# Performance work log

Measured on AMD Instinct MI355X. Metric: run time of the kernel, lower is better.

The kernel has to match this reference:

```python
import jax, jax.numpy as jnp
import numpy as np

B, D, HGT, WID = 32, 512, 8, 32   # batch, channels, feature map H, W
T = HGT * WID                     # 256 spatial tokens
NH, L, MAXLEN = 8, 2, 25          # heads, encoder layers, max text len


def _ln(x, s, b, eps=1e-5):
    m = jnp.mean(x, -1, keepdims=True)
    v = jnp.mean((x - m) ** 2, -1, keepdims=True)
    return (x - m) * jax.lax.rsqrt(v + eps) * s + b


def setup_inputs() -> dict:
    key = jax.random.key(0)
    ks = jax.random.split(key, 16)
    w = lambda k, shp: jax.random.normal(k, shp, jnp.float32) * 0.02
    return {
        "x": jax.random.normal(ks[0], (B, D, HGT, WID), jnp.float32),
        "encoder_word_pos": jnp.arange(T, dtype=jnp.int32),
        "gsrm_word_pos": jnp.arange(MAXLEN, dtype=jnp.int32),
        # encoder positional table
        "pos_table": w(ks[1], (T, D)),
        # per-layer encoder params (stacked over L)
        "ln1_s": jnp.ones((L, D), jnp.float32), "ln1_b": jnp.zeros((L, D), jnp.float32),
        "Wq": w(ks[2], (L, D, D)), "bq": jnp.zeros((L, D), jnp.float32),
        "Wk": w(ks[3], (L, D, D)), "bk": jnp.zeros((L, D), jnp.float32),
        "Wv": w(ks[4], (L, D, D)), "bv": jnp.zeros((L, D), jnp.float32),
        "Wo": w(ks[5], (L, D, D)), "bo": jnp.zeros((L, D), jnp.float32),
        "ln2_s": jnp.ones((L, D), jnp.float32), "ln2_b": jnp.zeros((L, D), jnp.float32),
        "W1": w(ks[6], (L, D, D)), "b1": jnp.zeros((L, D), jnp.float32),  # d_inner_hid = hidden_dim
        "W2": w(ks[7], (L, D, D)), "b2": jnp.zeros((L, D), jnp.float32),
        "lnf_s": jnp.ones((D,), jnp.float32), "lnf_b": jnp.zeros((D,), jnp.float32),
        # PVAM head params
        "fc0_w": w(ks[8], (D, D)), "fc0_b": jnp.zeros((D,), jnp.float32),
        "emb_table": w(ks[9], (MAXLEN, D)),
        "fc1_w": w(ks[10], (D,)),
    }


def _pvam(x, encoder_word_pos, gsrm_word_pos, pos_table,
          ln1_s, ln1_b, Wq, bq, Wk, bk, Wv, bv, Wo, bo,
          ln2_s, ln2_b, W1, b1, W2, b2, lnf_s, lnf_b,
          fc0_w, fc0_b, emb_table, fc1_w):
    b, c, h, wd = x.shape
    feat = x.reshape(b, c, h * wd).transpose(0, 2, 1)          # [b, t, c]
    # prepare encoder: scale + learned positional embedding (eval mode: no dropout)
    enc = feat * jnp.sqrt(jnp.float32(c)) + pos_table[encoder_word_pos]
    dk = c // NH
    scale = 1.0 / jnp.sqrt(jnp.float32(dk))
    for l in range(L):  # pre-norm transformer encoder (preprocess='n', postprocess='da')
        qin = _ln(enc, ln1_s[l], ln1_b[l])
        q = (qin @ Wq[l] + bq[l]).reshape(b, -1, NH, dk)
        k = (qin @ Wk[l] + bk[l]).reshape(b, -1, NH, dk)
        v = (qin @ Wv[l] + bv[l]).reshape(b, -1, NH, dk)
        p = jax.nn.softmax(jnp.einsum('bqhd,bkhd->bhqk', q, k) * scale, -1)
        o = jnp.einsum('bhqk,bkhd->bqhd', p, v).reshape(b, -1, c)
        enc = enc + (o @ Wo[l] + bo[l])
        y = _ln(enc, ln2_s[l], ln2_b[l])
        enc = enc + (jax.nn.relu(y @ W1[l] + b1[l]) @ W2[l] + b2[l])
    enc = _ln(enc, lnf_s, lnf_b)
    word_features = enc @ fc0_w + fc0_b                        # [b, t, c]
    word_pos = emb_table[gsrm_word_pos]                        # [max_len, c]
    # additive attention: tanh(broadcast add) -> scalar score -> softmax over t
    y = jnp.tanh(word_features[:, None, :, :] + word_pos[None, :, None, :])  # [b,max_len,t,c]
    attn = jax.nn.softmax(jnp.einsum('bmtc,c->bmt', y, fc1_w), -1)
    return jnp.einsum('bmt,btc->bmc', attn, word_features)    # [b, max_len, c]


def reference(x, encoder_word_pos, gsrm_word_pos, pos_table,
              ln1_s, ln1_b, Wq, bq, Wk, bk, Wv, bv, Wo, bo,
              ln2_s, ln2_b, W1, b1, W2, b2, lnf_s, lnf_b,
              fc0_w, fc0_b, emb_table, fc1_w):
    return _pvam(x, encoder_word_pos, gsrm_word_pos, pos_table,
                 ln1_s, ln1_b, Wq, bq, Wk, bk, Wv, bv, Wo, bo,
                 ln2_s, ln2_b, W1, b1, W2, b2, lnf_s, lnf_b,
                 fc0_w, fc0_b, emb_table, fc1_w)
```

## Files before the change

### kernel.cpp

```cpp
#include <hip/hip_runtime.h>
#include <math.h>

#define B_ 32
#define D_ 512
#define T_ 256
#define NH_ 8
#define DK_ 64
#define ML_ 25

typedef unsigned short ushort_t;
using short8 = __attribute__((ext_vector_type(8))) short;
using f32x4  = __attribute__((ext_vector_type(4))) float;

__device__ __forceinline__ ushort_t f2bf(float f) {
    unsigned u = __float_as_uint(f);
    unsigned r = (u + 0x7fffu + ((u >> 16) & 1u)) >> 16;
    return (ushort_t)r;
}
__device__ __forceinline__ float bf2f(ushort_t h) {
    return __uint_as_float(((unsigned)h) << 16);
}
__device__ __forceinline__ void gl16(const void* g, void* l) {
    __builtin_amdgcn_global_load_lds((const __attribute__((address_space(1))) void*)g,
                                     (__attribute__((address_space(3))) void*)l, 16, 0, 0);
}
#define ZERO4(v) { (v)[0]=0.f; (v)[1]=0.f; (v)[2]=0.f; (v)[3]=0.f; }

__global__ __launch_bounds__(256) void prep_kernel(const float* __restrict__ x,
                                                   const int* __restrict__ epos,
                                                   const float* __restrict__ pos,
                                                   float* __restrict__ enc) {
    __shared__ float ld[64][65];
    int tt = blockIdx.x, ct = blockIdx.y, b = blockIdx.z;
    int t0 = tt * 64, c0 = ct * 64;
    int tid = threadIdx.x;
    int r = tid >> 4, c4 = (tid & 15) << 2;
#pragma unroll
    for (int p = 0; p < 4; p++) {
        int row = p * 16 + r;
        float4 v = *(const float4*)(x + ((size_t)(b * D_ + c0 + row) * T_ + t0) + c4);
        ld[row][c4 + 0] = v.x; ld[row][c4 + 1] = v.y; ld[row][c4 + 2] = v.z; ld[row][c4 + 3] = v.w;
    }
    __syncthreads();
#pragma unroll
    for (int p = 0; p < 4; p++) {
        int tr = p * 16 + r;
        int ep = epos[t0 + tr];
        float4 pv = *(const float4*)(pos + (size_t)ep * D_ + c0 + c4);
        float4 o;
        o.x = ld[c4 + 0][tr] * 22.627417f + pv.x;
        o.y = ld[c4 + 1][tr] * 22.627417f + pv.y;
        o.z = ld[c4 + 2][tr] * 22.627417f + pv.z;
        o.w = ld[c4 + 3][tr] * 22.627417f + pv.w;
        *(float4*)(enc + (size_t)(b * T_ + t0 + tr) * D_ + c0 + c4) = o;
    }
}

__global__ __launch_bounds__(256) void convert_w_kernel(const float* __restrict__ Wq,
                                                        const float* __restrict__ Wk,
                                                        const float* __restrict__ Wv,
                                                        const float* __restrict__ Wo,
                                                        const float* __restrict__ W1,
                                                        const float* __restrict__ W2,
                                                        const float* __restrict__ fc0,
                                                        ushort_t* __restrict__ wt) {
    __shared__ float ld[64][65];
    int m = blockIdx.x >> 6;
    int tile = blockIdx.x & 63;
    int tn = tile >> 3, tk = tile & 7;
    int n0 = tn * 64, k0 = tk * 64;
    const float* src;
    if (m < 12) {
        int l = m / 6, w = m % 6;
        const float* bases[6] = {Wq, Wk, Wv, Wo, W1, W2};
        src = bases[w] + (size_t)l * D_ * D_;
    } else {
        src = fc0;
    }
    int tid = threadIdx.x;
    int r = tid >> 4, c4 = (tid & 15) << 2;
#pragma unroll
    for (int p = 0; p < 4; p++) {
        int row = p * 16 + r;
        float4 v = *(const float4*)(src + (size_t)(k0 + row) * D_ + n0 + c4);
        ld[row][c4 + 0] = v.x; ld[row][c4 + 1] = v.y; ld[row][c4 + 2] = v.z; ld[row][c4 + 3] = v.w;
    }
    __syncthreads();
    ushort_t* dsth = wt + (size_t)m * D_ * D_;
    ushort_t* dstl = wt + (size_t)13 * D_ * D_;
#pragma unroll
    for (int p = 0; p < 4; p++) {
        int n = p * 16 + r;
        int kc = c4;
        ushort_t h[4], lo[4];
#pragma unroll
        for (int i = 0; i < 4; i++) {
            float f = ld[kc + i][n];
            h[i] = f2bf(f);
            lo[i] = f2bf(f - bf2f(h[i]));
        }
        *(ushort4*)(dsth + (size_t)(n0 + n) * D_ + k0 + kc) = make_ushort4(h[0], h[1], h[2], h[3]);
        if (m == 12)
            *(ushort4*)(dstl + (size_t)(n0 + n) * D_ + k0 + kc) = make_ushort4(lo[0], lo[1], lo[2], lo[3]);
    }
}

template<bool LO>
__global__ __launch_bounds__(256) void ln_kernel(const float* __restrict__ x,
                                                 const float* __restrict__ s,
                                                 const float* __restrict__ b,
                                                 ushort_t* __restrict__ yh,
                                                 ushort_t* __restrict__ yl) {
    int wid = threadIdx.x >> 6, lane = threadIdx.x & 63;
    size_t row = (size_t)blockIdx.x * 4 + wid;
    const float4* xr = (const float4*)(x + row * D_);
    float4 v0 = xr[lane * 2], v1 = xr[lane * 2 + 1];
    float sum = v0.x + v0.y + v0.z + v0.w + v1.x + v1.y + v1.z + v1.w;
    for (int o = 32; o; o >>= 1) sum += __shfl_xor(sum, o);
    float mean = sum * (1.f / 512.f);
    float d[8] = {v0.x - mean, v0.y - mean, v0.z - mean, v0.w - mean,
                  v1.x - mean, v1.y - mean, v1.z - mean, v1.w - mean};
    float vs = 0.f;
#pragma unroll
    for (int i = 0; i < 8; i++) vs += d[i] * d[i];
    for (int o = 32; o; o >>= 1) vs += __shfl_xor(vs, o);
    float rs = 1.f / sqrtf(vs * (1.f / 512.f) + 1e-5f);
    const float4* s4 = (const float4*)s;
    const float4* b4 = (const float4*)b;
    float4 sa = s4[lane * 2], sb = s4[lane * 2 + 1];
    float4 ba = b4[lane * 2], bb = b4[lane * 2 + 1];
    float o8[8];
    o8[0] = d[0] * rs * sa.x + ba.x; o8[1] = d[1] * rs * sa.y + ba.y;
    o8[2] = d[2] * rs * sa.z + ba.z; o8[3] = d[3] * rs * sa.w + ba.w;
    o8[4] = d[4] * rs * sb.x + bb.x; o8[5] = d[5] * rs * sb.y + bb.y;
    o8[6] = d[6] * rs * sb.z + bb.z; o8[7] = d[7] * rs * sb.w + bb.w;
    ushort_t h[8];
#pragma unroll
    for (int i = 0; i < 8; i++) h[i] = f2bf(o8[i]);
    uint4 u;
    u.x = (unsigned)h[0] | ((unsigned)h[1] << 16);
    u.y = (unsigned)h[2] | ((unsigned)h[3] << 16);
    u.z = (unsigned)h[4] | ((unsigned)h[5] << 16);
    u.w = (unsigned)h[6] | ((unsigned)h[7] << 16);
    *(uint4*)(yh + row * D_ + lane * 8) = u;
    if (LO) {
        ushort_t l8[8];
#pragma unroll
        for (int i = 0; i < 8; i++) l8[i] = f2bf(o8[i] - bf2f(h[i]));
        uint4 ul;
        ul.x = (unsigned)l8[0] | ((unsigned)l8[1] << 16);
        ul.y = (unsigned)l8[2] | ((unsigned)l8[3] << 16);
        ul.z = (unsigned)l8[4] | ((unsigned)l8[5] << 16);
        ul.w = (unsigned)l8[6] | ((unsigned)l8[7] << 16);
        *(uint4*)(yl + row * D_ + lane * 8) = ul;
    }
}

template<int EPI>
__global__ __launch_bounds__(256) void gemm_kernel(const ushort_t* __restrict__ A0,
                                                   const ushort_t* __restrict__ A1,
                                                   const ushort_t* __restrict__ A2,
                                                   const ushort_t* __restrict__ B0,
                                                   const ushort_t* __restrict__ B1,
                                                   const ushort_t* __restrict__ B2,
                                                   int nseg, int nbn,
                                                   const float* __restrict__ bias,
                                                   const float* __restrict__ bias2,
                                                   const float* __restrict__ bias3,
                                                   const float* __restrict__ res,
                                                   float* __restrict__ outF,
                                                   ushort_t* __restrict__ outB) {
    __shared__ ushort_t As[3][64 * 64];
    __shared__ ushort_t Bs[3][64 * 64];
    int tid = threadIdx.x;
    int g = blockIdx.x;
    int per = gridDim.x >> 3;
    int lin = (g & 7) * per + (g >> 3);
    int bm = lin / nbn, bn = lin % nbn;

    int lane = tid & 63;
    int wid = tid >> 6;
    int wm = wid >> 1, wn = wid & 1;
    int xr = (lane & 7) << 3;

    f32x4 acc[2][2];
#pragma unroll
    for (int i = 0; i < 2; i++)
#pragma unroll
        for (int j = 0; j < 2; j++) ZERO4(acc[i][j]);

    int nt = nseg * 8;

#define STAGE(kt, buf)                                                                  \
    {                                                                                   \
        int seg_ = (kt) >> 3;                                                           \
        int k0_ = ((kt) & 7) * 64;                                                      \
        const ushort_t* Asg = seg_ == 0 ? A0 : (seg_ == 1 ? A1 : A2);                   \
        const ushort_t* Bsg = seg_ == 0 ? B0 : (seg_ == 1 ? B1 : B2);                   \
        _Pragma("unroll")                                                               \
        for (int it = 0; it < 2; it++) {                                                \
            int uu = tid + it * 256;                                                    \
            int row_ = uu >> 3;                                                         \
            int kb_ = (((uu & 7) ^ (row_ & 7)) << 3);                                   \
            gl16(Asg + (size_t)(bm * 64 + row_) * 512 + k0_ + kb_, &As[buf][uu * 8]);   \
        }                                                                               \
        _Pragma("unroll")                                                               \
        for (int it = 0; it < 2; it++) {                                                \
            int uu = tid + it * 256;                                                    \
            int row_ = uu >> 3;                                                         \
            int kb_ = (((uu & 7) ^ (row_ & 7)) << 3);                                   \
            gl16(Bsg + (size_t)(bn * 64 + row_) * 512 + k0_ + kb_, &Bs[buf][uu * 8]);   \
        }                                                                               \
    }

#define COMPUTE(bufc)                                                                        \
    {                                                                                        \
        _Pragma("unroll")                                                                    \
        for (int kc = 0; kc < 2; kc++) {                                                     \
            short8 a[2], b[2];                                                               \
            int koff = (kc * 32 + ((lane >> 4) << 3)) ^ xr;                                  \
            _Pragma("unroll")                                                                \
            for (int i = 0; i < 2; i++)                                                      \
                a[i] = *(const short8*)&As[bufc][(wm * 32 + i * 16 + (lane & 15)) * 64 + koff]; \
            _Pragma("unroll")                                                                \
            for (int j = 0; j < 2; j++)                                                      \
                b[j] = *(const short8*)&Bs[bufc][(wn * 32 + j * 16 + (lane & 15)) * 64 + koff]; \
            _Pragma("unroll")                                                                \
            for (int i = 0; i < 2; i++)                                                      \
                _Pragma("unroll")                                                            \
                for (int j = 0; j < 2; j++)                                                  \
                    acc[i][j] = __builtin_amdgcn_mfma_f32_16x16x32_bf16(a[i], b[j], acc[i][j], 0, 0, 0); \
        }                                                                                    \
    }

    STAGE(0, 0);
    STAGE(1, 1);
    asm volatile("s_waitcnt vmcnt(4)" ::: "memory");
    __builtin_amdgcn_s_barrier();

    int cur = 0;
    for (int t = 0; t < nt; t++) {
        if (t + 2 < nt) STAGE(t + 2, (cur + 2 >= 3 ? cur - 1 : cur + 2));
        COMPUTE(cur);
        if (t + 2 < nt) {
            asm volatile("s_waitcnt vmcnt(4)" ::: "memory");
        } else if (t + 1 < nt) {
            asm volatile("s_waitcnt vmcnt(0)" ::: "memory");
        }
        __builtin_amdgcn_s_barrier();
        cur = (cur == 2) ? 0 : cur + 1;
    }
#undef STAGE
#undef COMPUTE

#pragma unroll
    for (int i = 0; i < 2; i++) {
#pragma unroll
        for (int j = 0; j < 2; j++) {
            int r0 = bm * 64 + wm * 32 + i * 16 + ((lane >> 4) << 2);
            int col = bn * 64 + wn * 32 + j * 16 + (lane & 15);
            int seg = col >> 9;
            int ccol = col & 511;
            const float* bp = bias;
            if (EPI == 5) bp = (seg == 0) ? bias : (seg == 1 ? bias2 : bias3);
            float bc = bp[EPI == 5 ? ccol : col];
#pragma unroll
            for (int jj = 0; jj < 4; jj++) {
                float v = acc[i][j][jj] + bc;
                int row = r0 + jj;
                size_t idx = (size_t)row * 512 + col;
                if (EPI == 2) {
                    outF[idx] = v + res[idx];
                } else if (EPI == 3) {
                    outB[idx] = f2bf(fmaxf(v, 0.f));
                } else if (EPI == 4) {
                    outF[idx] = v;
                } else if (EPI == 5) {
                    if (seg < 2) {
                        outB[(size_t)seg * 4194304 + (size_t)row * 512 + ccol] = f2bf(v);
                    } else {
                        int bb2 = row >> 8, t2 = row & 255;
                        outB[(size_t)2 * 4194304 +
                             ((size_t)(bb2 * 8 + (ccol >> 6)) * 64 + (ccol & 63)) * 256 + t2] = f2bf(v);
                    }
                }
            }
        }
    }
}

__global__ __launch_bounds__(256) void attn_fused_kernel(const ushort_t* __restrict__ q,
                                                         const ushort_t* __restrict__ k,
                                                         const ushort_t* __restrict__ vt,
                                                         ushort_t* __restrict__ ao) {
    __shared__ ushort_t KVs[256 * 64];
    __shared__ ushort_t Ps[64 * 256];
    int tid = threadIdx.x;
    int lane = tid & 63;
    int wid = tid >> 6;
    int m0 = blockIdx.x * 64;
    int bh = blockIdx.y;
    int b = bh >> 3, h = bh & 7;
    int xr = (lane & 7) << 3;

#pragma unroll
    for (int it = 0; it < 8; it++) {
        int uu = tid + it * 256;
        int row = uu >> 3;
        int gx = ((uu & 7) ^ (row & 7)) << 3;
        gl16(k + (size_t)(b * T_ + row) * D_ + h * DK_ + gx, &KVs[uu * 8]);
    }
    short8 qa0, qa1;
    {
        int qrow = m0 + wid * 16 + (lane & 15);
        const ushort_t* qp = q + (size_t)(b * T_ + qrow) * D_ + h * DK_ + ((lane >> 4) << 3);
        qa0 = *(const short8*)(qp);
        qa1 = *(const short8*)(qp + 32);
    }
    f32x4 acc[16];
#pragma unroll
    for (int j = 0; j < 16; j++) ZERO4(acc[j]);
    asm volatile("s_waitcnt vmcnt(0)" ::: "memory");
    __syncthreads();

#pragma unroll
    for (int j = 0; j < 16; j++) {
        int krow = j * 16 + (lane & 15);
        short8 b0 = *(const short8*)&KVs[krow * 64 + ((((lane >> 4) << 3)) ^ xr)];
        short8 b1 = *(const short8*)&KVs[krow * 64 + ((32 + ((lane >> 4) << 3)) ^ xr)];
        acc[j] = __builtin_amdgcn_mfma_f32_16x16x32_bf16(qa0, b0, acc[j], 0, 0, 0);
        acc[j] = __builtin_amdgcn_mfma_f32_16x16x32_bf16(qa1, b1, acc[j], 0, 0, 0);
    }
    __syncthreads();

#pragma unroll
    for (int it = 0; it < 8; it++) {
        int uu = tid + it * 256;
        int row = uu >> 5;
        int gx = ((uu & 31) ^ (row & 7)) << 3;
        gl16(vt + ((size_t)bh * DK_ + row) * T_ + gx, &KVs[uu * 8]);
    }

    const float C = 0.125f * 1.44269504f;
#pragma unroll
    for (int jj = 0; jj < 4; jj++) {
        float mx = -1e30f;
#pragma unroll
        for (int j = 0; j < 16; j++) mx = fmaxf(mx, acc[j][jj]);
#pragma unroll
        for (int msk = 1; msk < 16; msk <<= 1) mx = fmaxf(mx, __shfl_xor(mx, msk));
        float sm = 0.f;
#pragma unroll
        for (int j = 0; j < 16; j++) {
            float e = __builtin_amdgcn_exp2f((acc[j][jj] - mx) * C);
            acc[j][jj] = e;
            sm += e;
        }
#pragma unroll
        for (int msk = 1; msk < 16; msk <<= 1) sm += __shfl_xor(sm, msk);
        float inv = 1.f / sm;
#pragma unroll
        for (int j = 0; j < 16; j++) acc[j][jj] *= inv;
    }
#pragma unroll
    for (int j = 0; j < 16; j++) {
#pragma unroll
        for (int jj = 0; jj < 4; jj++) {
            int row = wid * 16 + ((lane >> 4) << 2) + jj;
            int col = j * 16 + (lane & 15);
            Ps[row * 256 + (col ^ ((row & 7) << 3))] = f2bf(acc[j][jj]);
        }
    }
    asm volatile("s_waitcnt vmcnt(0)" ::: "memory");
    __syncthreads();

    int wm = wid >> 1, wn = wid & 1;
    f32x4 acc2[2][2];
#pragma unroll
    for (int i = 0; i < 2; i++)
#pragma unroll
        for (int j = 0; j < 2; j++) ZERO4(acc2[i][j]);
#pragma unroll
    for (int kc = 0; kc < 8; kc++) {
        int off = (kc * 32 + ((lane >> 4) << 3)) ^ xr;
        short8 a0 = *(const short8*)&Ps[(wm * 32 + (lane & 15)) * 256 + off];
        short8 a1 = *(const short8*)&Ps[(wm * 32 + 16 + (lane & 15)) * 256 + off];
        short8 b0 = *(const short8*)&KVs[(wn * 32 + (lane & 15)) * 256 + off];
        short8 b1 = *(const short8*)&KVs[(wn * 32 + 16 + (lane & 15)) * 256 + off];
        acc2[0][0] = __builtin_amdgcn_mfma_f32_16x16x32_bf16(a0, b0, acc2[0][0], 0, 0, 0);
        acc2[0][1] = __builtin_amdgcn_mfma_f32_16x16x32_bf16(a0, b1, acc2[0][1], 0, 0, 0);
        acc2[1][0] = __builtin_amdgcn_mfma_f32_16x16x32_bf16(a1, b0, acc2[1][0], 0, 0, 0);
        acc2[1][1] = __builtin_amdgcn_mfma_f32_16x16x32_bf16(a1, b1, acc2[1][1], 0, 0, 0);
    }
#pragma unroll
    for (int i = 0; i < 2; i++)
#pragma unroll
        for (int j = 0; j < 2; j++)
#pragma unroll
            for (int jj = 0; jj < 4; jj++)
                ao[(size_t)(b * T_ + m0 + wm * 32 + i * 16 + ((lane >> 4) << 2) + jj) * D_ +
                   h * DK_ + wn * 32 + j * 16 + (lane & 15)] = f2bf(acc2[i][j][jj]);
}

__global__ __launch_bounds__(256) void scores_kernel(const float* __restrict__ wf,
                                                     const int* __restrict__ gpos,
                                                     const float* __restrict__ emb,
                                                     const float* __restrict__ w1,
                                                     float* __restrict__ scores) {
    __shared__ float wpL[5][512];
    __shared__ float w1m2[512];
    const float K2 = 2.885390082f;
    int tid = threadIdx.x;
    int b = blockIdx.y;
    int mg = blockIdx.z * 5;
    int t = blockIdx.x * 32 + (tid >> 3);
    int cg = tid & 7;
    for (int idx = tid; idx < 5 * 128; idx += 256) {
        int m = idx >> 7, w4 = idx & 127;
        float4 v = *(const float4*)(emb + (size_t)gpos[mg + m] * D_ + (w4 << 2));
        v.x *= K2; v.y *= K2; v.z *= K2; v.w *= K2;
        *(float4*)&wpL[m][w4 << 2] = v;
    }
    if (tid < 128) {
        float4 v = *(const float4*)(w1 + (tid << 2));
        v.x *= -2.f; v.y *= -2.f; v.z *= -2.f; v.w *= -2.f;
        *(float4*)&w1m2[tid << 2] = v;
    }
    float4 wfs[16];
    float W1S = 0.f;
    const float* wfr = wf + (size_t)(b * T_ + t) * D_ + (cg << 2);
#pragma unroll
    for (int j = 0; j < 16; j++) {
        float4 v = *(const float4*)(wfr + (j << 5));
        wfs[j].x = v.x * K2; wfs[j].y = v.y * K2; wfs[j].z = v.z * K2; wfs[j].w = v.w * K2;
        float4 wv = *(const float4*)(w1 + (cg << 2) + (j << 5));
        W1S += wv.x + wv.y + wv.z + wv.w;
    }
    __syncthreads();
    float s[5] = {W1S, W1S, W1S, W1S, W1S};
#pragma unroll
    for (int j = 0; j < 16; j++) {
        float4 w14 = *(const float4*)&w1m2[(cg << 2) + (j << 5)];
#pragma unroll
        for (int m = 0; m < 5; m++) {
            float4 wp4 = *(const float4*)&wpL[m][(cg << 2) + (j << 5)];
            s[m] += w14.x * __builtin_amdgcn_rcpf(__builtin_amdgcn_exp2f(wfs[j].x + wp4.x) + 1.f);
            s[m] += w14.y * __builtin_amdgcn_rcpf(__builtin_amdgcn_exp2f(wfs[j].y + wp4.y) + 1.f);
            s[m] += w14.z * __builtin_amdgcn_rcpf(__builtin_amdgcn_exp2f(wfs[j].z + wp4.z) + 1.f);
            s[m] += w14.w * __builtin_amdgcn_rcpf(__builtin_amdgcn_exp2f(wfs[j].w + wp4.w) + 1.f);
        }
    }
#pragma unroll
    for (int m = 0; m < 5; m++) {
        s[m] += __shfl_xor(s[m], 1);
        s[m] += __shfl_xor(s[m], 2);
        s[m] += __shfl_xor(s[m], 4);
    }
    if (cg == 0) {
#pragma unroll
        for (int m = 0; m < 5; m++)
            scores[((size_t)b * ML_ + mg + m) * T_ + t] = s[m];
    }
}

__global__ __launch_bounds__(256) void wsum_kernel(const float* __restrict__ scores,
                                                   const float* __restrict__ wf,
                                                   float* __restrict__ out) {
    __shared__ float at[T_][8];
    __shared__ float redmax[4][8];
    __shared__ float redsum[4][8];
    int tid = threadIdx.x;
    int lane = tid & 63, wv = tid >> 6;
    int b = blockIdx.y, m0 = blockIdx.x * 5;
    float s[5];
#pragma unroll
    for (int q = 0; q < 5; q++)
        s[q] = scores[((size_t)b * ML_ + m0 + q) * T_ + tid];
#pragma unroll
    for (int q = 0; q < 5; q++) {
        float mx = s[q];
        for (int o = 32; o; o >>= 1) mx = fmaxf(mx, __shfl_xor(mx, o));
        if (lane == 0) redmax[wv][q] = mx;
    }
    __syncthreads();
    float e[5];
#pragma unroll
    for (int q = 0; q < 5; q++) {
        float m = fmaxf(fmaxf(redmax[0][q], redmax[1][q]), fmaxf(redmax[2][q], redmax[3][q]));
        e[q] = __expf(s[q] - m);
        float sm = e[q];
        for (int o = 32; o; o >>= 1) sm += __shfl_xor(sm, o);
        if (lane == 0) redsum[wv][q] = sm;
    }
    __syncthreads();
#pragma unroll
    for (int q = 0; q < 5; q++) {
        float sm = redsum[0][q] + redsum[1][q] + redsum[2][q] + redsum[3][q];
        at[tid][q] = e[q] / sm;
    }
    __syncthreads();
    int c0 = tid << 1;
    const float* wfb = wf + (size_t)b * T_ * D_ + c0;
    float acc[5][2] = {};
    for (int t = 0; t < T_; t++) {
        float2 v = *(const float2*)(wfb + (size_t)t * D_);
        float4 a4 = *(const float4*)&at[t][0];
        float a5 = at[t][4];
        acc[0][0] += a4.x * v.x; acc[0][1] += a4.x * v.y;
        acc[1][0] += a4.y * v.x; acc[1][1] += a4.y * v.y;
        acc[2][0] += a4.z * v.x; acc[2][1] += a4.z * v.y;
        acc[3][0] += a4.w * v.x; acc[3][1] += a4.w * v.y;
        acc[4][0] += a5 * v.x;   acc[4][1] += a5 * v.y;
    }
#pragma unroll
    for (int q = 0; q < 5; q++) {
        float2 o;
        o.x = acc[q][0]; o.y = acc[q][1];
        *(float2*)(out + ((size_t)b * ML_ + m0 + q) * D_ + c0) = o;
    }
}

extern "C" void kernel_launch(void* const* d_in, const int* in_sizes, int n_in,
                              void* d_out, int out_size, void* d_ws, size_t ws_size,
                              hipStream_t stream) {
    (void)in_sizes; (void)n_in; (void)out_size; (void)ws_size;
    const float* x        = (const float*)d_in[0];
    const int*   epos     = (const int*)d_in[1];
    const int*   gpos     = (const int*)d_in[2];
    const float* pos_tab  = (const float*)d_in[3];
    const float* ln1_s    = (const float*)d_in[4];
    const float* ln1_b    = (const float*)d_in[5];
    const float* Wq       = (const float*)d_in[6];
    const float* bq       = (const float*)d_in[7];
    const float* Wk       = (const float*)d_in[8];
    const float* bk       = (const float*)d_in[9];
    const float* Wv       = (const float*)d_in[10];
    const float* bv       = (const float*)d_in[11];
    const float* Wo       = (const float*)d_in[12];
    const float* bo       = (const float*)d_in[13];
    const float* ln2_s    = (const float*)d_in[14];
    const float* ln2_b    = (const float*)d_in[15];
    const float* W1       = (const float*)d_in[16];
    const float* b1       = (const float*)d_in[17];
    const float* W2       = (const float*)d_in[18];
    const float* b2       = (const float*)d_in[19];
    const float* lnf_s    = (const float*)d_in[20];
    const float* lnf_b    = (const float*)d_in[21];
    const float* fc0_w    = (const float*)d_in[22];
    const float* fc0_b    = (const float*)d_in[23];
    const float* emb      = (const float*)d_in[24];
    const float* fc1_w    = (const float*)d_in[25];

    char* ws = (char*)d_ws;
    float*    enc = (float*)(ws);
    ushort_t* hi  = (ushort_t*)(ws + 16777216);
    ushort_t* qb  = (ushort_t*)(ws + 25165824);
    ushort_t* kb  = (ushort_t*)(ws + 33554432);
    ushort_t* lo  = (ushort_t*)(ws + 33554432);
    float*    scb = (float*)(ws + 33554432);
    ushort_t* vt  = (ushort_t*)(ws + 41943040);
    ushort_t* h1  = (ushort_t*)(ws + 41943040);
    ushort_t* ao  = (ushort_t*)(ws + 50331648);
    float*    wf  = (float*)(ws + 58720256);
    ushort_t* wt  = (ushort_t*)(ws + 75497472);
    const size_t WSL = (size_t)D_ * D_;

    convert_w_kernel<<<13 * 64, 256, 0, stream>>>(Wq, Wk, Wv, Wo, W1, W2, fc0_w, wt);
    prep_kernel<<<dim3(4, 8, 32), 256, 0, stream>>>(x, epos, pos_tab, enc);

    for (int l = 0; l < 2; l++) {
        size_t o1 = (size_t)l * D_;
        const ushort_t* WqkvT = wt + (l * 6 + 0) * WSL;
        const ushort_t* WoT = wt + (l * 6 + 3) * WSL;
        const ushort_t* W1T = wt + (l * 6 + 4) * WSL;
        const ushort_t* W2T = wt + (l * 6 + 5) * WSL;

        ln_kernel<false><<<2048, 256, 0, stream>>>(enc, ln1_s + o1, ln1_b + o1, hi, nullptr);
        gemm_kernel<5><<<3072, 256, 0, stream>>>(hi, nullptr, nullptr, WqkvT, nullptr, nullptr,
                                                 1, 24, bq + o1, bk + o1, bv + o1, nullptr, nullptr, qb);
        attn_fused_kernel<<<dim3(4, 256), 256, 0, stream>>>(qb, kb, vt, ao);
        gemm_kernel<2><<<1024, 256, 0, stream>>>(ao, nullptr, nullptr, WoT, nullptr, nullptr,
                                                 1, 8, bo + o1, nullptr, nullptr, enc, enc, nullptr);
        ln_kernel<false><<<2048, 256, 0, stream>>>(enc, ln2_s + o1, ln2_b + o1, hi, nullptr);
        gemm_kernel<3><<<1024, 256, 0, stream>>>(hi, nullptr, nullptr, W1T, nullptr, nullptr,
                                                 1, 8, b1 + o1, nullptr, nullptr, nullptr, nullptr, h1);
        gemm_kernel<2><<<1024, 256, 0, stream>>>(h1, nullptr, nullptr, W2T, nullptr, nullptr,
                                                 1, 8, b2 + o1, nullptr, nullptr, enc, enc, nullptr);
    }

    ln_kernel<true><<<2048, 256, 0, stream>>>(enc, lnf_s, lnf_b, hi, lo);
    gemm_kernel<4><<<1024, 256, 0, stream>>>(hi, lo, hi, wt + 12 * WSL, wt + 12 * WSL, wt + 13 * WSL,
                                             3, 8, fc0_b, nullptr, nullptr, nullptr, wf, nullptr);
    scores_kernel<<<dim3(8, 32, 5), 256, 0, stream>>>(wf, gpos, emb, fc1_w, scb);
    wsum_kernel<<<dim3(5, 32), 256, 0, stream>>>(scb, wf, (float*)d_out);
}
```

Baseline: 313.1 us.

## Enlarge GEMM tiles to 128-row blocks and add dedicated 128x128 QKV kernel

The generic GEMM tile grows from 64x64 to 128x64, so each wave computes 64x32 outputs and the grid is halved. A new QKV projection kernel uses 128x128 tiles with double buffering and keeps the bias selection and V-transpose epilogue. Larger tiles raise reuse of each loaded operand and cut global and LDS traffic per FLOP. In exchange they use more LDS and registers per block and launch fewer blocks, which may lower occupancy and leave fewer blocks to spread across CUs.

```diff
diff --git a/kernel.cpp b/kernel.cpp
--- a/kernel.cpp
+++ b/kernel.cpp
@@ -165,12 +165,10 @@
                                                    const ushort_t* __restrict__ B2,
                                                    int nseg, int nbn,
                                                    const float* __restrict__ bias,
-                                                   const float* __restrict__ bias2,
-                                                   const float* __restrict__ bias3,
                                                    const float* __restrict__ res,
                                                    float* __restrict__ outF,
                                                    ushort_t* __restrict__ outB) {
-    __shared__ ushort_t As[3][64 * 64];
+    __shared__ ushort_t As[3][128 * 64];
     __shared__ ushort_t Bs[3][64 * 64];
     int tid = threadIdx.x;
     int g = blockIdx.x;
@@ -183,9 +181,9 @@
     int wm = wid >> 1, wn = wid & 1;
     int xr = (lane & 7) << 3;
 
-    f32x4 acc[2][2];
-#pragma unroll
-    for (int i = 0; i < 2; i++)
+    f32x4 acc[4][2];
+#pragma unroll
+    for (int i = 0; i < 4; i++)
 #pragma unroll
         for (int j = 0; j < 2; j++) ZERO4(acc[i][j]);
 
@@ -198,11 +196,11 @@
         const ushort_t* Asg = seg_ == 0 ? A0 : (seg_ == 1 ? A1 : A2);                   \
         const ushort_t* Bsg = seg_ == 0 ? B0 : (seg_ == 1 ? B1 : B2);                   \
         _Pragma("unroll")                                                               \
-        for (int it = 0; it < 2; it++) {                                                \
+        for (int it = 0; it < 4; it++) {                                                \
             int uu = tid + it * 256;                                                    \
             int row_ = uu >> 3;                                                         \
             int kb_ = (((uu & 7) ^ (row_ & 7)) << 3);                                   \
-            gl16(Asg + (size_t)(bm * 64 + row_) * 512 + k0_ + kb_, &As[buf][uu * 8]);   \
+            gl16(Asg + (size_t)(bm * 128 + row_) * 512 + k0_ + kb_, &As[buf][uu * 8]);  \
         }                                                                               \
         _Pragma("unroll")                                                               \
         for (int it = 0; it < 2; it++) {                                                \
@@ -217,16 +215,16 @@
     {                                                                                        \
         _Pragma("unroll")                                                                    \
         for (int kc = 0; kc < 2; kc++) {                                                     \
-            short8 a[2], b[2];                                                               \
+            short8 a[4], b[2];                                                               \
             int koff = (kc * 32 + ((lane >> 4) << 3)) ^ xr;                                  \
             _Pragma("unroll")                                                                \
-            for (int i = 0; i < 2; i++)                                                      \
-                a[i] = *(const short8*)&As[bufc][(wm * 32 + i * 16 + (lane & 15)) * 64 + koff]; \
+            for (int i = 0; i < 4; i++)                                                      \
+                a[i] = *(const short8*)&As[bufc][(wm * 64 + i * 16 + (lane & 15)) * 64 + koff]; \
             _Pragma("unroll")                                                                \
             for (int j = 0; j < 2; j++)                                                      \
                 b[j] = *(const short8*)&Bs[bufc][(wn * 32 + j * 16 + (lane & 15)) * 64 + koff]; \
             _Pragma("unroll")                                                                \
-            for (int i = 0; i < 2; i++)                                                      \
+            for (int i = 0; i < 4; i++)                                                      \
                 _Pragma("unroll")                                                            \
                 for (int j = 0; j < 2; j++)                                                  \
                     acc[i][j] = __builtin_amdgcn_mfma_f32_16x16x32_bf16(a[i], b[j], acc[i][j], 0, 0, 0); \
@@ -234,8 +232,8 @@
     }
 
     STAGE(0, 0);
-    STAGE(1, 1);
-    asm volatile("s_waitcnt vmcnt(4)" ::: "memory");
+    if (nt > 1) STAGE(1, 1);
+    asm volatile("s_waitcnt vmcnt(6)" ::: "memory");
     __builtin_amdgcn_s_barrier();
 
     int cur = 0;
@@ -243,7 +241,7 @@
         if (t + 2 < nt) STAGE(t + 2, (cur + 2 >= 3 ? cur - 1 : cur + 2));
         COMPUTE(cur);
         if (t + 2 < nt) {
-            asm volatile("s_waitcnt vmcnt(4)" ::: "memory");
+            asm volatile("s_waitcnt vmcnt(6)" ::: "memory");
         } else if (t + 1 < nt) {
             asm volatile("s_waitcnt vmcnt(0)" ::: "memory");
         }
@@ -254,16 +252,12 @@
 #undef COMPUTE
 
 #pragma unroll
-    for (int i = 0; i < 2; i++) {
+    for (int i = 0; i < 4; i++) {
 #pragma unroll
         for (int j = 0; j < 2; j++) {
-            int r0 = bm * 64 + wm * 32 + i * 16 + ((lane >> 4) << 2);
+            int r0 = bm * 128 + wm * 64 + i * 16 + ((lane >> 4) << 2);
             int col = bn * 64 + wn * 32 + j * 16 + (lane & 15);
-            int seg = col >> 9;
-            int ccol = col & 511;
-            const float* bp = bias;
-            if (EPI == 5) bp = (seg == 0) ? bias : (seg == 1 ? bias2 : bias3);
-            float bc = bp[EPI == 5 ? ccol : col];
+            float bc = bias[col];
 #pragma unroll
             for (int jj = 0; jj < 4; jj++) {
                 float v = acc[i][j][jj] + bc;
@@ -273,16 +267,101 @@
                     outF[idx] = v + res[idx];
                 } else if (EPI == 3) {
                     outB[idx] = f2bf(fmaxf(v, 0.f));
-                } else if (EPI == 4) {
+                } else {
                     outF[idx] = v;
-                } else if (EPI == 5) {
-                    if (seg < 2) {
-                        outB[(size_t)seg * 4194304 + (size_t)row * 512 + ccol] = f2bf(v);
-                    } else {
-                        int bb2 = row >> 8, t2 = row & 255;
-                        outB[(size_t)2 * 4194304 +
-                             ((size_t)(bb2 * 8 + (ccol >> 6)) * 64 + (ccol & 63)) * 256 + t2] = f2bf(v);
-                    }
+                }
+            }
+        }
+    }
+}
+
+__global__ __launch_bounds__(256) void gemm_qkv_kernel(const ushort_t* __restrict__ A,
+                                                       const ushort_t* __restrict__ W,
+                                                       const float* __restrict__ bq,
+                                                       const float* __restrict__ bk,
+                                                       const float* __restrict__ bv,
+                                                       ushort_t* __restrict__ outB) {
+    __shared__ ushort_t As[2][128 * 64];
+    __shared__ ushort_t Bs[2][128 * 64];
+    int tid = threadIdx.x;
+    int g = blockIdx.x;
+    int per = gridDim.x >> 3;
+    int lin = (g & 7) * per + (g >> 3);
+    int bm = lin / 12, bn = lin % 12;
+
+    int lane = tid & 63;
+    int wid = tid >> 6;
+    int wm = wid >> 1, wn = wid & 1;
+    int xr = (lane & 7) << 3;
+
+    f32x4 acc[4][4];
+#pragma unroll
+    for (int i = 0; i < 4; i++)
+#pragma unroll
+        for (int j = 0; j < 4; j++) ZERO4(acc[i][j]);
+
+#define QSTAGE(kt, buf)                                                                 \
+    {                                                                                   \
+        int k0_ = (kt) * 64;                                                            \
+        _Pragma("unroll")                                                               \
+        for (int it = 0; it < 4; it++) {                                                \
+            int uu = tid + it * 256;                                                    \
+            int row_ = uu >> 3;                                                         \
+            int kb_ = (((uu & 7) ^ (row_ & 7)) << 3);                                   \
+            gl16(A + (size_t)(bm * 128 + row_) * 512 + k0_ + kb_, &As[buf][uu * 8]);    \
+            gl16(W + (size_t)(bn * 128 + row_) * 512 + k0_ + kb_, &Bs[buf][uu * 8]);    \
+        }                                                                               \
+    }
+
+    QSTAGE(0, 0);
+    asm volatile("s_waitcnt vmcnt(0)" ::: "memory");
+    __builtin_amdgcn_s_barrier();
+
+    int buf = 0;
+    for (int t = 0; t < 8; t++) {
+        if (t + 1 < 8) QSTAGE(t + 1, buf ^ 1);
+#pragma unroll
+        for (int kc = 0; kc < 2; kc++) {
+            short8 a[4], b[4];
+            int koff = (kc * 32 + ((lane >> 4) << 3)) ^ xr;
+#pragma unroll
+            for (int i = 0; i < 4; i++)
+                a[i] = *(const short8*)&As[buf][(wm * 64 + i * 16 + (lane & 15)) * 64 + koff];
+#pragma unroll
+            for (int j = 0; j < 4; j++)
+                b[j] = *(const short8*)&Bs[buf][(wn * 64 + j * 16 + (lane & 15)) * 64 + koff];
+#pragma unroll
+            for (int i = 0; i < 4; i++)
+#pragma unroll
+                for (int j = 0; j < 4; j++)
+                    acc[i][j] = __builtin_amdgcn_mfma_f32_16x16x32_bf16(a[i], b[j], acc[i][j], 0, 0, 0);
+        }
+        if (t + 1 < 8) asm volatile("s_waitcnt vmcnt(0)" ::: "memory");
+        __builtin_amdgcn_s_barrier();
+        buf ^= 1;
+    }
+#undef QSTAGE
+
+#pragma unroll
+    for (int i = 0; i < 4; i++) {
+#pragma unroll
+        for (int j = 0; j < 4; j++) {
+            int r0 = bm * 128 + wm * 64 + i * 16 + ((lane >> 4) << 2);
+            int col = bn * 128 + wn * 64 + j * 16 + (lane & 15);
+            int seg = col >> 9;
+            int ccol = col & 511;
+            const float* bp = (seg == 0) ? bq : (seg == 1 ? bk : bv);
+            float bc = bp[ccol];
+#pragma unroll
+            for (int jj = 0; jj < 4; jj++) {
+                float v = acc[i][j][jj] + bc;
+                int row = r0 + jj;
+                if (seg < 2) {
+                    outB[(size_t)seg * 4194304 + (size_t)row * 512 + ccol] = f2bf(v);
+                } else {
+                    int bb2 = row >> 8, t2 = row & 255;
+                    outB[(size_t)2 * 4194304 +
+                         ((size_t)(bb2 * 8 + (ccol >> 6)) * 64 + (ccol & 63)) * 256 + t2] = f2bf(v);
                 }
             }
         }
@@ -576,21 +655,20 @@
         const ushort_t* W2T = wt + (l * 6 + 5) * WSL;
 
         ln_kernel<false><<<2048, 256, 0, stream>>>(enc, ln1_s + o1, ln1_b + o1, hi, nullptr);
-        gemm_kernel<5><<<3072, 256, 0, stream>>>(hi, nullptr, nullptr, WqkvT, nullptr, nullptr,
-                                                 1, 24, bq + o1, bk + o1, bv + o1, nullptr, nullptr, qb);
+        gemm_qkv_kernel<<<768, 256, 0, stream>>>(hi, WqkvT, bq + o1, bk + o1, bv + o1, qb);
         attn_fused_kernel<<<dim3(4, 256), 256, 0, stream>>>(qb, kb, vt, ao);
-        gemm_kernel<2><<<1024, 256, 0, stream>>>(ao, nullptr, nullptr, WoT, nullptr, nullptr,
-                                                 1, 8, bo + o1, nullptr, nullptr, enc, enc, nullptr);
+        gemm_kernel<2><<<512, 256, 0, stream>>>(ao, nullptr, nullptr, WoT, nullptr, nullptr,
+                                                1, 8, bo + o1, enc, enc, nullptr);
         ln_kernel<false><<<2048, 256, 0, stream>>>(enc, ln2_s + o1, ln2_b + o1, hi, nullptr);
-        gemm_kernel<3><<<1024, 256, 0, stream>>>(hi, nullptr, nullptr, W1T, nullptr, nullptr,
-                                                 1, 8, b1 + o1, nullptr, nullptr, nullptr, nullptr, h1);
-        gemm_kernel<2><<<1024, 256, 0, stream>>>(h1, nullptr, nullptr, W2T, nullptr, nullptr,
-                                                 1, 8, b2 + o1, nullptr, nullptr, enc, enc, nullptr);
+        gemm_kernel<3><<<512, 256, 0, stream>>>(hi, nullptr, nullptr, W1T, nullptr, nullptr,
+                                                1, 8, b1 + o1, nullptr, nullptr, h1);
+        gemm_kernel<2><<<512, 256, 0, stream>>>(h1, nullptr, nullptr, W2T, nullptr, nullptr,
+                                                1, 8, b2 + o1, enc, enc, nullptr);
     }
 
     ln_kernel<true><<<2048, 256, 0, stream>>>(enc, lnf_s, lnf_b, hi, lo);
-    gemm_kernel<4><<<1024, 256, 0, stream>>>(hi, lo, hi, wt + 12 * WSL, wt + 12 * WSL, wt + 13 * WSL,
-                                             3, 8, fc0_b, nullptr, nullptr, nullptr, wf, nullptr);
+    gemm_kernel<4><<<512, 256, 0, stream>>>(hi, lo, hi, wt + 12 * WSL, wt + 12 * WSL, wt + 13 * WSL,
+                                            3, 8, fc0_b, nullptr, wf, nullptr);
     scores_kernel<<<dim3(8, 32, 5), 256, 0, stream>>>(wf, gpos, emb, fc1_w, scb);
     wsum_kernel<<<dim3(5, 32), 256, 0, stream>>>(scb, wf, (float*)d_out);
 }
```

Result: faster. 295.0 us (-5.8%).
